# Kernel optimization log

Measured on AMD Instinct MI355X. Metric: run time of the kernel, lower is better.

The kernel has to match this reference:

```python
import jax, jax.numpy as jnp
import numpy as np
import math

B = 2
D_MODEL = 2048
L_MAX = 4096
FILTER_ORDER = 64
EMB_DIM = 3
SHORT_K = 3


def setup_inputs() -> dict:
    key = jax.random.key(0)
    ks = jax.random.split(key, 16)
    D = D_MODEL

    def n(k, shape, scale=0.02):
        return jax.random.normal(k, shape, dtype=jnp.float32) * scale

    return {
        "x": jax.random.normal(ks[0], (B, L_MAX, D), dtype=jnp.float32),
        "in_proj_w": n(ks[1], (3 * D, D)),
        "in_proj_b": n(ks[2], (3 * D,)),
        "short_w": n(ks[3], (3 * D, 1, SHORT_K), 0.3),   # depthwise conv weight (O, I/groups=1, K)
        "short_b": n(ks[4], (3 * D,), 0.1),
        "mlp_w0": n(ks[5], (FILTER_ORDER, EMB_DIM), 0.5),
        "mlp_b0": n(ks[6], (FILTER_ORDER,), 0.5),
        "sin_freq": jnp.ones((1, FILTER_ORDER), dtype=jnp.float32),  # Sin module, w=1, shared across MLP layers
        "mlp_w1": n(ks[7], (FILTER_ORDER, FILTER_ORDER), 0.1),
        "mlp_b1": n(ks[8], (FILTER_ORDER,), 0.1),
        "mlp_w2": n(ks[9], (FILTER_ORDER, FILTER_ORDER), 0.1),
        "mlp_b2": n(ks[10], (FILTER_ORDER,), 0.1),
        "mlp_w3": n(ks[11], (D, FILTER_ORDER), 0.1),      # final Linear(order -> d_model, bias=False)
        "filter_bias": jax.random.normal(ks[12], (D,), dtype=jnp.float32),  # HyenaFilter.bias ~ randn
        "out_proj_w": n(ks[13], (D, D)),
        "out_proj_b": n(ks[14], (D,)),
    }


def _pos_emb(L):
    # PositionalEmbedding: t in [0,1], 1 complex band (emb_dim=3 -> bands=1)
    t = jnp.linspace(0.0, 1.0, L)[:, None]               # (L, 1)
    t_resc = jnp.linspace(0.0, L - 1.0, L)
    w = 2.0 * math.pi * t_resc / L                       # (L,)
    bands = (EMB_DIM - 1) // 2
    f = jnp.linspace(1e-4, bands - 1.0, bands)           # (bands,)
    ang = f[None, :] * w[:, None]                        # (L, bands)
    # z = exp(-1j * f * w) -> real = cos, imag = -sin
    z = jnp.concatenate([t, jnp.cos(ang), -jnp.sin(ang)], axis=-1)  # (L, 3)
    return z, t


def _filter_k(L, w0, b0, freq, w1, b1, w2, b2, w3):
    z, t = _pos_emb(L)
    h = jnp.sin(freq * (z @ w0.T + b0))
    h = jnp.sin(freq * (h @ w1.T + b1))
    h = jnp.sin(freq * (h @ w2.T + b2))
    h = h @ w3.T                                         # (L, D)
    # ExponentialModulation: deltas = linspace(log(.01)/1.5, log(.01)/0.3, D)
    max_decay = math.log(0.01) / 0.3
    min_decay = math.log(0.01) / 1.5
    deltas = jnp.linspace(min_decay, max_decay, h.shape[-1])
    decay = jnp.exp(-t * jnp.abs(deltas)[None, :])       # (L, D)
    return (h * decay).T                                 # (D, L)


def _fftconv(u, k, bias):
    # fftconv_ref with gelu=False, no dropout_mask: u (B, D, L), k (D, L), bias (D,)
    L = u.shape[-1]
    n = 2 * L
    k_f = jnp.fft.rfft(k, n=n) / n                       # (D, L+1)
    u_f = jnp.fft.rfft(u, n=n)                           # (B, D, L+1)
    y = jnp.fft.irfft(u_f * k_f, n=n, norm="forward")[..., :L]
    return y + u * bias[:, None]


def reference(x, in_proj_w, in_proj_b, short_w, short_b, mlp_w0, mlp_b0, sin_freq,
              mlp_w1, mlp_b1, mlp_w2, mlp_b2, mlp_w3, filter_bias,
              out_proj_w, out_proj_b):
    Bn, L, D = x.shape
    u = x @ in_proj_w.T + in_proj_b                      # (B, L, 3D)
    u = jnp.transpose(u, (0, 2, 1))                      # (B, 3D, L)
    # depthwise short conv, padding = short_k - 1, truncate to L (causal-ish)
    uc = jax.lax.conv_general_dilated(
        u, short_w, window_strides=(1,),
        padding=[(SHORT_K - 1, SHORT_K - 1)],
        feature_group_count=3 * D,
        dimension_numbers=("NCH", "OIH", "NCH"))
    uc = uc[..., :L] + short_b[None, :, None]
    x0, x1, v = jnp.split(uc, 3, axis=1)                 # each (B, D, L)
    k = _filter_k(L, mlp_w0, mlp_b0, sin_freq, mlp_w1, mlp_b1, mlp_w2, mlp_b2, mlp_w3)
    # order=2 Hyena recurrence: single gated long-conv step
    v = v * x1
    v = _fftconv(v, k, filter_bias)
    y = v * x0                                           # (B, D, L)
    y = jnp.transpose(y, (0, 2, 1))                      # (B, L, D)
    return y @ out_proj_w.T + out_proj_b
```

## Files before the change

### kernel.cpp

```cpp
#include <hip/hip_runtime.h>
#include <hip/hip_bf16.h>
#include <cstdint>
#include <cstddef>

typedef __attribute__((ext_vector_type(8))) short    bf16x8;
typedef __attribute__((ext_vector_type(4))) float    f32x4;
typedef __attribute__((ext_vector_type(8))) unsigned short u16x8;
typedef __attribute__((ext_vector_type(4))) float    f32v4;
typedef __attribute__((ext_vector_type(4))) unsigned short u16v4;

__device__ __forceinline__ float b2f(unsigned short v) {
    return __builtin_bit_cast(float, ((unsigned int)v) << 16);
}
__device__ __forceinline__ unsigned short f2b(float f) {
    unsigned int u = __builtin_bit_cast(unsigned int, f);
    u += 0x7fffu + ((u >> 16) & 1u);
    return (unsigned short)(u >> 16);
}

__device__ __forceinline__ void async16(const void* g, void* l) {
    __builtin_amdgcn_global_load_lds(
        (const __attribute__((address_space(1))) unsigned int*)g,
        (__attribute__((address_space(3))) unsigned int*)l, 16, 0, 0);
}

__global__ __launch_bounds__(256) void cvt2_f32_bf16(
    const float* __restrict__ srcA, unsigned short* __restrict__ dstA, int n4A,
    const float* __restrict__ srcB, unsigned short* __restrict__ dstB, int n4B) {
    int i = blockIdx.x * blockDim.x + threadIdx.x;
    int stride = gridDim.x * blockDim.x;
    const int nTot = n4A + n4B;
    for (; i < nTot; i += stride) {
        const bool inA = (i < n4A);
        const f32v4* s4 = inA ? (const f32v4*)srcA : (const f32v4*)srcB;
        u16v4* d4 = inA ? (u16v4*)dstA : (u16v4*)dstB;
        const int k = inA ? i : (i - n4A);
        f32v4 v = s4[k];
        u16v4 o;
        o.x = f2b(v.x); o.y = f2b(v.y); o.z = f2b(v.z); o.w = f2b(v.w);
        d4[k] = o;
    }
}

__global__ __launch_bounds__(256) void cvt_f32_bf16(const float* __restrict__ src,
                                                    unsigned short* __restrict__ dst, int n4) {
    int i = blockIdx.x * blockDim.x + threadIdx.x;
    int stride = gridDim.x * blockDim.x;
    const f32v4* s4 = (const f32v4*)src;
    u16v4* d4 = (u16v4*)dst;
    for (; i < n4; i += stride) {
        f32v4 v = s4[i];
        u16v4 o;
        o.x = f2b(v.x); o.y = f2b(v.y); o.z = f2b(v.z); o.w = f2b(v.w);
        d4[i] = o;
    }
}

template <int MODE>
__global__ __launch_bounds__(512, 1) void gemm256(
    const unsigned short* __restrict__ A,
    const unsigned short* __restrict__ Bw,
    const float* __restrict__ bias,
    void* __restrict__ Cout,
    int M, int N, int K, int Lseq, int CH, int ntn)
{
    constexpr int SMEM_BYTES = (MODE == 1) ? 135168 : 131072;
    __shared__ char smemc[SMEM_BYTES];

    const int tid = threadIdx.x;
    const int w   = tid >> 6;
    const int l   = tid & 63;
    const int wm  = w & 1;
    const int wn  = w >> 1;
    const int quad = l >> 4;
    const int lq   = l & 15;

    const int bid = blockIdx.x;
    const int x  = bid & 7;
    const int j  = bid >> 3;
    const int bx = (j & 7) + 8 * (j >> 5);
    const int by = (x << 2) | ((j >> 3) & 3);
    const int n0 = bx * 256, m0 = by * 256;

    const int su0 = quad ^ (lq & 7);
    const int su1 = su0 ^ 4;

    uint32_t offAe[2][2], offBe[2][2];
    int dA[2][2], dB[2][2];
    #pragma unroll
    for (int h = 0; h < 2; ++h)
        #pragma unroll
        for (int c = 0; c < 2; ++c) {
            const int Lr = h * 128 + w * 16 + c * 8 + (l >> 3);
            const int gA = ((Lr & 64) << 1) | ((Lr & 128) >> 1) | (Lr & 63);
            const int u  = (l & 7) ^ (l >> 3);
            offAe[h][c] = (uint32_t)(m0 + gA) * (uint32_t)K + (uint32_t)(u * 8);
            offBe[h][c] = (uint32_t)(n0 + Lr) * (uint32_t)K + (uint32_t)(u * 8);
            const int rb = (h * 128 + w * 16 + c * 8) * 128;
            dA[h][c] = rb;
            dB[h][c] = 32768 + rb;
        }

#define STAGE_A(bs, h, tile) do { \
    async16(A + offAe[h][0] + (size_t)(tile) * 64, smemc + ((bs) * 65536 + dA[h][0])); \
    async16(A + offAe[h][1] + (size_t)(tile) * 64, smemc + ((bs) * 65536 + dA[h][1])); \
} while (0)
#define STAGE_B(bs, h, tile) do { \
    async16(Bw + offBe[h][0] + (size_t)(tile) * 64, smemc + ((bs) * 65536 + dB[h][0])); \
    async16(Bw + offBe[h][1] + (size_t)(tile) * 64, smemc + ((bs) * 65536 + dB[h][1])); \
} while (0)

    f32x4 acc[8][4] = {};
    bf16x8 bw[4][2], a[2][2];

#define LDB8(bs) do { \
    _Pragma("unroll") for (int jj = 0; jj < 4; ++jj) { \
        const int Lr = wn * 64 + jj * 16 + lq; \
        bw[jj][0] = *(const bf16x8*)(smemc + (bs) * 65536 + 32768 + Lr * 128 + su0 * 16); \
        bw[jj][1] = *(const bf16x8*)(smemc + (bs) * 65536 + 32768 + Lr * 128 + su1 * 16); \
    } } while (0)
#define LDA4(bs, q) do { \
    _Pragma("unroll") for (int mf = 0; mf < 2; ++mf) { \
        const int g = wm * 128 + (q) * 32 + mf * 16 + lq; \
        const int Lr = ((g & 64) << 1) | ((g & 128) >> 1) | (g & 63); \
        a[mf][0] = *(const bf16x8*)(smemc + (bs) * 65536 + Lr * 128 + su0 * 16); \
        a[mf][1] = *(const bf16x8*)(smemc + (bs) * 65536 + Lr * 128 + su1 * 16); \
    } } while (0)
#define MFMA16(q) do { \
    _Pragma("unroll") for (int mf = 0; mf < 2; ++mf) \
    _Pragma("unroll") for (int jj = 0; jj < 4; ++jj) \
    _Pragma("unroll") for (int kk = 0; kk < 2; ++kk) \
        acc[(q) * 2 + mf][jj] = __builtin_amdgcn_mfma_f32_16x16x32_bf16(a[mf][kk], bw[jj][kk], acc[(q) * 2 + mf][jj], 0, 0, 0); \
} while (0)
#define PHASE_SYNC() do { \
    __builtin_amdgcn_s_barrier(); \
    asm volatile("s_waitcnt lgkmcnt(0)" ::: "memory"); \
    __builtin_amdgcn_sched_barrier(0); \
    __builtin_amdgcn_s_setprio(1); \
} while (0)
#define PHASE_END() do { \
    __builtin_amdgcn_s_setprio(0); \
    __builtin_amdgcn_s_barrier(); \
} while (0)
#define PHASE_END_DRAIN(lastf) do { \
    __builtin_amdgcn_s_setprio(0); \
    if (lastf) asm volatile("s_waitcnt vmcnt(0)" ::: "memory"); \
    else       asm volatile("s_waitcnt vmcnt(6)" ::: "memory"); \
    __builtin_amdgcn_s_barrier(); \
} while (0)

    STAGE_B(0, 0, 0); STAGE_B(0, 1, 0); STAGE_A(0, 0, 0); STAGE_A(0, 1, 0);
    STAGE_B(1, 0, 1); STAGE_B(1, 1, 1); STAGE_A(1, 0, 1);
    asm volatile("s_waitcnt vmcnt(6)" ::: "memory");
    __builtin_amdgcn_s_barrier();

    const int nIt = K >> 7;
    for (int i = 0; i < nIt; ++i) {
        const bool last = (i == nIt - 1);
        const int t0 = 2 * i, t1 = 2 * i + 1;
        LDB8(0); LDA4(0, 0); STAGE_A(1, 1, t1);
        PHASE_SYNC(); MFMA16(0); PHASE_END();
        LDA4(0, 1); if (!last) STAGE_B(0, 0, t0 + 2);
        PHASE_SYNC(); MFMA16(1); PHASE_END();
        LDA4(0, 2); if (!last) STAGE_B(0, 1, t0 + 2);
        PHASE_SYNC(); MFMA16(2); PHASE_END();
        LDA4(0, 3); if (!last) STAGE_A(0, 0, t0 + 2);
        PHASE_SYNC(); MFMA16(3); PHASE_END_DRAIN(last);
        LDB8(1); LDA4(1, 0); if (!last) STAGE_A(0, 1, t0 + 2);
        PHASE_SYNC(); MFMA16(0); PHASE_END();
        LDA4(1, 1); if (!last) STAGE_B(1, 0, t1 + 2);
        PHASE_SYNC(); MFMA16(1); PHASE_END();
        LDA4(1, 2); if (!last) STAGE_B(1, 1, t1 + 2);
        PHASE_SYNC(); MFMA16(2); PHASE_END();
        LDA4(1, 3); if (!last) STAGE_A(1, 0, t1 + 2);
        PHASE_SYNC(); MFMA16(3); PHASE_END_DRAIN(last);
    }

    if (MODE == 0) {
        float* out = (float*)Cout;
        #pragma unroll
        for (int jj = 0; jj < 4; ++jj) {
            const int col = n0 + wn * 64 + jj * 16 + lq;
            const float bv = bias[col];
            #pragma unroll
            for (int i8 = 0; i8 < 8; ++i8) {
                const int rowb = m0 + wm * 128 + i8 * 16 + quad * 4;
                f32x4 c = acc[i8][jj];
                out[(size_t)(rowb + 0) * N + col] = c.x + bv;
                out[(size_t)(rowb + 1) * N + col] = c.y + bv;
                out[(size_t)(rowb + 2) * N + col] = c.z + bv;
                out[(size_t)(rowb + 3) * N + col] = c.w + bv;
            }
        }
    } else {
        unsigned short* sE = (unsigned short*)smemc;
        __syncthreads();
        #pragma unroll
        for (int jj = 0; jj < 4; ++jj) {
            const int nl = wn * 64 + jj * 16 + lq;
            const float bv = bias[n0 + nl];
            #pragma unroll
            for (int i8 = 0; i8 < 8; ++i8) {
                const int ml = wm * 128 + i8 * 16 + quad * 4;
                f32x4 c = acc[i8][jj];
                u16v4 pk;
                pk.x = f2b(c.x + bv); pk.y = f2b(c.y + bv);
                pk.z = f2b(c.z + bv); pk.w = f2b(c.w + bv);
                *(u16v4*)&sE[nl * 264 + ml] = pk;
            }
        }
        __syncthreads();
        unsigned short* uo = (unsigned short*)Cout;
        const int bI = m0 >> 12;
        const int l0 = m0 & 4095;
        for (int e = tid; e < 8192; e += 512) {
            const int nl = e >> 5, seg = e & 31;
            u16x8 v = *(const u16x8*)&sE[nl * 264 + seg * 8];
            *(u16x8*)&uo[(size_t)(bI * CH + n0 + nl) * Lseq + l0 + seg * 8] = v;
        }
    }
#undef STAGE_A
#undef STAGE_B
#undef LDB8
#undef LDA4
#undef MFMA16
#undef PHASE_SYNC
#undef PHASE_END
#undef PHASE_END_DRAIN
}

__global__ __launch_bounds__(256) void filter_kernel(
    const float* __restrict__ w0, const float* __restrict__ b0,
    const float* __restrict__ freq,
    const float* __restrict__ w1, const float* __restrict__ b1,
    const float* __restrict__ w2, const float* __restrict__ b2,
    const float* __restrict__ w3, float* __restrict__ kf)
{
    __shared__ float ha[64][64];
    __shared__ float hb[64][64];
    const int tid = threadIdx.x;
    const int l0 = blockIdx.x * 64;
    const int d0 = blockIdx.y * 256;
    const int l  = tid & 63;
    const int lg = l0 + l;
    const float tt = (float)lg * (1.0f / 4095.0f);
    const float wang = 6.283185307179586f * (float)lg * (1.0f / 4096.0f);
    const float a  = 1e-4f * wang;
    const float z0 = tt, z1 = cosf(a), z2 = -sinf(a);

    for (int e = tid; e < 4096; e += 256) {
        const int dim = e >> 6;
        float pre = z0 * w0[dim * 3] + z1 * w0[dim * 3 + 1] + z2 * w0[dim * 3 + 2] + b0[dim];
        ha[dim][l] = sinf(freq[dim] * pre);
    }
    __syncthreads();
    for (int e = tid; e < 4096; e += 256) {
        const int dim = e >> 6;
        float acc = b1[dim];
        #pragma unroll
        for (int jj = 0; jj < 64; ++jj) acc += w1[dim * 64 + jj] * ha[jj][l];
        hb[dim][l] = sinf(freq[dim] * acc);
    }
    __syncthreads();
    for (int e = tid; e < 4096; e += 256) {
        const int dim = e >> 6;
        float acc = b2[dim];
        #pragma unroll
        for (int jj = 0; jj < 64; ++jj) acc += w2[dim * 64 + jj] * hb[jj][l];
        ha[dim][l] = sinf(freq[dim] * acc);
    }
    __syncthreads();
    for (int d = d0 + (tid >> 6); d < d0 + 256; d += 4) {
        float acc = 0.f;
        #pragma unroll
        for (int jj = 0; jj < 64; ++jj) acc += w3[d * 64 + jj] * ha[jj][l];
        const float delta = fabsf(-3.0701134573253944f + (-5.999245642062483e-3f) * (float)d);
        kf[(size_t)d * 4096 + lg] = acc * __expf(-tt * delta);
    }
}

#define PIDX(i) ((i) + (((i) >> 5) << 2))

__device__ __forceinline__ void bfly_f(float& r1, float& i1, float& r2, float& i2, float wr, float wi) {
    float ur = r1, ui = i1, vr = r2, vi = i2;
    r1 = ur + vr; i1 = ui + vi;
    float dr = ur - vr, di = ui - vi;
    r2 = dr * wr - di * wi;
    i2 = dr * wi + di * wr;
}
__device__ __forceinline__ void bfly_i(float& r1, float& i1, float& r2, float& i2, float wr, float wi) {
    float vr = r2 * wr - i2 * wi, vi = r2 * wi + i2 * wr;
    float ur = r1, ui = i1;
    r1 = ur + vr; i1 = ui + vi;
    r2 = ur - vr; i2 = ui - vi;
}

template <int DS, int STR>
__device__ __forceinline__ void fwd_stage(float* re, float* im, int tt) {
    float wr[8], wi[8];
    constexpr float c = -3.14159265358979f / (float)(STR * DS);
    #pragma unroll
    for (int k = 0; k < DS; ++k) __sincosf(c * (float)(tt + STR * k), &wi[k], &wr[k]);
    #pragma unroll
    for (int s = 0; s < 16; ++s)
        if ((s & DS) == 0)
            bfly_f(re[s], im[s], re[s + DS], im[s + DS], wr[s & (DS - 1)], wi[s & (DS - 1)]);
}
template <int DS, int STR>
__device__ __forceinline__ void inv_stage(float* re, float* im, int tt) {
    float wr[8], wi[8];
    constexpr float c = 3.14159265358979f / (float)(STR * DS);
    #pragma unroll
    for (int k = 0; k < DS; ++k) __sincosf(c * (float)(tt + STR * k), &wi[k], &wr[k]);
    #pragma unroll
    for (int s = 0; s < 16; ++s)
        if ((s & DS) == 0)
            bfly_i(re[s], im[s], re[s + DS], im[s + DS], wr[s & (DS - 1)], wi[s & (DS - 1)]);
}

__device__ constexpr float TW8C[8] = { 1.f,  0.9238795325112867f,  0.7071067811865476f,  0.3826834323650898f,
                                       0.f, -0.3826834323650898f, -0.7071067811865476f, -0.9238795325112867f };
__device__ constexpr float TW8S[8] = { 0.f,  0.3826834323650898f,  0.7071067811865476f,  0.9238795325112867f,
                                       1.f,  0.9238795325112867f,  0.7071067811865476f,  0.3826834323650898f };
template <int DS>
__device__ __forceinline__ void fwd_stageC(float* re, float* im) {
    #pragma unroll
    for (int s = 0; s < 16; ++s)
        if ((s & DS) == 0) {
            const int k = (s & (DS - 1)) * (8 / DS);
            bfly_f(re[s], im[s], re[s + DS], im[s + DS], TW8C[k], -TW8S[k]);
        }
}
template <int DS>
__device__ __forceinline__ void inv_stageC(float* re, float* im) {
    #pragma unroll
    for (int s = 0; s < 16; ++s)
        if ((s & DS) == 0) {
            const int k = (s & (DS - 1)) * (8 / DS);
            bfly_i(re[s], im[s], re[s + DS], im[s + DS], TW8C[k], TW8S[k]);
        }
}

__device__ __forceinline__ void xchg(float* re, float* im, float* fre, float* fim,
                                     int wbase, int wstr, int rbase, int rstr) {
    __syncthreads();
    if (wstr == 1) {
        #pragma unroll
        for (int q = 0; q < 4; ++q) {
            f32x4 vr, vi;
            vr.x = re[4*q+0]; vr.y = re[4*q+1]; vr.z = re[4*q+2]; vr.w = re[4*q+3];
            vi.x = im[4*q+0]; vi.y = im[4*q+1]; vi.z = im[4*q+2]; vi.w = im[4*q+3];
            *(f32x4*)&fre[PIDX(wbase + 4*q)] = vr;
            *(f32x4*)&fim[PIDX(wbase + 4*q)] = vi;
        }
    } else {
        #pragma unroll
        for (int s = 0; s < 16; ++s) {
            const int i = wbase + wstr * s;
            fre[PIDX(i)] = re[s]; fim[PIDX(i)] = im[s];
        }
    }
    __syncthreads();
    if (rstr == 1) {
        #pragma unroll
        for (int q = 0; q < 4; ++q) {
            f32x4 vr = *(const f32x4*)&fre[PIDX(rbase + 4*q)];
            f32x4 vi = *(const f32x4*)&fim[PIDX(rbase + 4*q)];
            re[4*q+0] = vr.x; re[4*q+1] = vr.y; re[4*q+2] = vr.z; re[4*q+3] = vr.w;
            im[4*q+0] = vi.x; im[4*q+1] = vi.y; im[4*q+2] = vi.z; im[4*q+3] = vi.w;
        }
    } else {
        #pragma unroll
        for (int s = 0; s < 16; ++s) {
            const int i = rbase + rstr * s;
            re[s] = fre[PIDX(i)]; im[s] = fim[PIDX(i)];
        }
    }
}

__device__ __forceinline__ void fwd_fft(float* re, float* im, float* fre, float* fim, int t) {
    const int off = t & 31, seg = t >> 5;
    fwd_stage<8, 512>(re, im, t);
    fwd_stage<4, 512>(re, im, t);
    fwd_stage<2, 512>(re, im, t);
    fwd_stage<1, 512>(re, im, t);
    xchg(re, im, fre, fim, t, 512, seg * 512 + off, 32);
    fwd_stage<8, 32>(re, im, off);
    fwd_stage<4, 32>(re, im, off);
    fwd_stage<2, 32>(re, im, off);
    fwd_stage<1, 32>(re, im, off);
    {
        float wr, wi;
        __sincosf(-3.14159265358979f * (float)(off & 15) / 16.0f, &wi, &wr);
        const bool hi = (off & 16) != 0;
        #pragma unroll
        for (int s = 0; s < 16; ++s) {
            float rr = __shfl_xor(re[s], 16);
            float ri = __shfl_xor(im[s], 16);
            if (!hi) { re[s] += rr; im[s] += ri; }
            else {
                float dr = rr - re[s], di = ri - im[s];
                re[s] = dr * wr - di * wi;
                im[s] = dr * wi + di * wr;
            }
        }
    }
    xchg(re, im, fre, fim, seg * 512 + off, 32, 16 * t, 1);
    fwd_stageC<8>(re, im);
    fwd_stageC<4>(re, im);
    fwd_stageC<2>(re, im);
    fwd_stageC<1>(re, im);
}

__device__ __forceinline__ void inv_fft(float* re, float* im, float* fre, float* fim, int t) {
    const int off = t & 31, seg = t >> 5;
    inv_stageC<1>(re, im);
    inv_stageC<2>(re, im);
    inv_stageC<4>(re, im);
    inv_stageC<8>(re, im);
    xchg(re, im, fre, fim, 16 * t, 1, seg * 512 + off, 32);
    {
        float wr, wi;
        __sincosf(3.14159265358979f * (float)(off & 15) / 16.0f, &wi, &wr);
        const bool hi = (off & 16) != 0;
        #pragma unroll
        for (int s = 0; s < 16; ++s) {
            float rr = __shfl_xor(re[s], 16);
            float ri = __shfl_xor(im[s], 16);
            if (!hi) {
                float vr = rr * wr - ri * wi, vi = rr * wi + ri * wr;
                re[s] += vr; im[s] += vi;
            } else {
                float vr = re[s] * wr - im[s] * wi, vi = re[s] * wi + im[s] * wr;
                re[s] = rr - vr; im[s] = ri - vi;
            }
        }
    }
    inv_stage<1, 32>(re, im, off);
    inv_stage<2, 32>(re, im, off);
    inv_stage<4, 32>(re, im, off);
    inv_stage<8, 32>(re, im, off);
    xchg(re, im, fre, fim, seg * 512 + off, 32, t, 512);
    inv_stage<1, 512>(re, im, t);
    inv_stage<2, 512>(re, im, t);
    inv_stage<4, 512>(re, im, t);
    inv_stage<8, 512>(re, im, t);
}

struct ConvPre { u16x8 v; float m1, m2; };
__device__ __forceinline__ ConvPre conv_pre(const unsigned short* __restrict__ row, int lb) {
    ConvPre p;
    p.v  = *(const u16x8*)(row + lb);
    p.m1 = (lb >= 1) ? b2f(row[lb - 1]) : 0.f;
    p.m2 = (lb >= 2) ? b2f(row[lb - 2]) : 0.f;
    return p;
}
__device__ __forceinline__ void conv_do(const ConvPre& p,
                                        float W0, float W1, float W2, float BB,
                                        float* __restrict__ out) {
    float f[8];
    #pragma unroll
    for (int j = 0; j < 8; ++j) f[j] = b2f((unsigned short)p.v[j]);
    out[0] = W0 * p.m2 + W1 * p.m1 + W2 * f[0] + BB;
    out[1] = W0 * p.m1 + W1 * f[0] + W2 * f[1] + BB;
    #pragma unroll
    for (int j = 2; j < 8; ++j) out[j] = W0 * f[j - 2] + W1 * f[j - 1] + W2 * f[j] + BB;
}

__global__ __launch_bounds__(512, 2) void hyena_fft_kernel(
    const unsigned short* __restrict__ u,
    const float* __restrict__ kf,
    const float* __restrict__ sw,
    const float* __restrict__ sbv,
    const float* __restrict__ fbias,
    unsigned short* __restrict__ zb)
{
    __shared__ __align__(16) float fre[9216];
    __shared__ __align__(16) float fim[9216];
    const int t = threadIdx.x;
    const int d = blockIdx.x;
    const int lb = t << 3;

    const int c0 = d, c1 = 2048 + d, c2 = 4096 + d;
    const float w10 = sw[c1*3+0], w11 = sw[c1*3+1], w12 = sw[c1*3+2], bb1 = sbv[c1];
    const float w20 = sw[c2*3+0], w21 = sw[c2*3+1], w22 = sw[c2*3+2], bb2 = sbv[c2];
    const float fb = fbias[d];

    ConvPre p1[2], p2[2];
    #pragma unroll
    for (int b = 0; b < 2; ++b) {
        const size_t base = (size_t)b * 6144 * 4096;
        p1[b] = conv_pre(u + base + (size_t)c1 * 4096, lb);
        p2[b] = conv_pre(u + base + (size_t)c2 * 4096, lb);
    }

    float kr[16], ki[16];
    #pragma unroll
    for (int s = 0; s < 16; ++s) {
        kr[s] = (s < 8) ? kf[(size_t)d * 4096 + t + 512 * s] : 0.f;
        ki[s] = 0.f;
    }
    fwd_fft(kr, ki, fre, fim, t);

    float vgc[2][8];
    #pragma unroll
    for (int b = 0; b < 2; ++b) {
        float e_[8], g_[8];
        conv_do(p1[b], w10, w11, w12, bb1, e_);
        conv_do(p2[b], w20, w21, w22, bb2, g_);
        #pragma unroll
        for (int j = 0; j < 8; ++j) vgc[b][j] = g_[j] * e_[j];
    }

    __syncthreads();
    #pragma unroll
    for (int q = 0; q < 2; ++q) {
        f32x4 vr, vi;
        vr.x = vgc[0][4*q+0]; vr.y = vgc[0][4*q+1]; vr.z = vgc[0][4*q+2]; vr.w = vgc[0][4*q+3];
        vi.x = vgc[1][4*q+0]; vi.y = vgc[1][4*q+1]; vi.z = vgc[1][4*q+2]; vi.w = vgc[1][4*q+3];
        *(f32x4*)&fre[PIDX(lb + 4*q)] = vr;
        *(f32x4*)&fim[PIDX(lb + 4*q)] = vi;
    }
    __syncthreads();
    float xr[16], xi[16];
    #pragma unroll
    for (int s = 0; s < 8; ++s) {
        xr[s] = fre[PIDX(t + (s << 9))];
        xi[s] = fim[PIDX(t + (s << 9))];
    }
    #pragma unroll
    for (int s = 8; s < 16; ++s) { xr[s] = 0.f; xi[s] = 0.f; }

    fwd_fft(xr, xi, fre, fim, t);
    #pragma unroll
    for (int j = 0; j < 16; ++j) {
        const float cr = xr[j], ci = xi[j];
        xr[j] = cr * kr[j] - ci * ki[j];
        xi[j] = cr * ki[j] + ci * kr[j];
    }

    ConvPre p0[2];
    #pragma unroll
    for (int b = 0; b < 2; ++b)
        p0[b] = conv_pre(u + (size_t)b * 6144 * 4096 + (size_t)c0 * 4096, lb);

    inv_fft(xr, xi, fre, fim, t);

    __syncthreads();
    #pragma unroll
    for (int s = 0; s < 8; ++s) {
        fre[PIDX(t + (s << 9))] = xr[s];
        fim[PIDX(t + (s << 9))] = xi[s];
    }
    __syncthreads();
    float yr[8], yi[8];
    #pragma unroll
    for (int q = 0; q < 2; ++q) {
        f32x4 vr = *(const f32x4*)&fre[PIDX(lb + 4*q)];
        f32x4 vi = *(const f32x4*)&fim[PIDX(lb + 4*q)];
        yr[4*q+0] = vr.x; yr[4*q+1] = vr.y; yr[4*q+2] = vr.z; yr[4*q+3] = vr.w;
        yi[4*q+0] = vi.x; yi[4*q+1] = vi.y; yi[4*q+2] = vi.z; yi[4*q+3] = vi.w;
    }
    const float w00 = sw[c0*3+0], w01 = sw[c0*3+1], w02 = sw[c0*3+2], bb0 = sbv[c0];
    const float inv_n = 1.0f / 8192.0f;
    #pragma unroll
    for (int b = 0; b < 2; ++b) {
        float a_[8];
        conv_do(p0[b], w00, w01, w02, bb0, a_);
        const float* Y = (b == 0) ? yr : yi;
        u16x8 zv;
        #pragma unroll
        for (int j = 0; j < 8; ++j)
            zv[j] = (unsigned short)f2b((Y[j] * inv_n + vgc[b][j] * fb) * a_[j]);
        *(u16x8*)&zb[(size_t)(b * 2048 + d) * 4096 + lb] = zv;
    }
}

__global__ __launch_bounds__(256) void transpose_kernel(const unsigned short* __restrict__ zb,
                                                        unsigned short* __restrict__ zt)
{
    __shared__ unsigned int tile[64][65];
    const int l0 = blockIdx.x * 64, d0 = blockIdx.y * 64, b = blockIdx.z;
    const int tid = threadIdx.x;
    for (int e = tid; e < 4096; e += 256) {
        const int r = e >> 6, c = e & 63;
        tile[r][c] = zb[(size_t)(b * 2048 + d0 + r) * 4096 + l0 + c];
    }
    __syncthreads();
    for (int e = tid; e < 4096; e += 256) {
        const int r = e >> 6, c = e & 63;
        zt[(size_t)(b * 4096 + l0 + r) * 2048 + d0 + c] = (unsigned short)tile[c][r];
    }
}

extern "C" void kernel_launch(void* const* d_in, const int* in_sizes, int n_in,
                              void* d_out, int out_size, void* d_ws, size_t ws_size,
                              hipStream_t stream)
{
    const float* x   = (const float*)d_in[0];
    const float* ipw = (const float*)d_in[1];
    const float* ipb = (const float*)d_in[2];
    const float* sw  = (const float*)d_in[3];
    const float* sb  = (const float*)d_in[4];
    const float* w0  = (const float*)d_in[5];
    const float* b0  = (const float*)d_in[6];
    const float* fr  = (const float*)d_in[7];
    const float* w1  = (const float*)d_in[8];
    const float* b1  = (const float*)d_in[9];
    const float* w2  = (const float*)d_in[10];
    const float* b2  = (const float*)d_in[11];
    const float* w3  = (const float*)d_in[12];
    const float* fb  = (const float*)d_in[13];
    const float* opw = (const float*)d_in[14];
    const float* opb = (const float*)d_in[15];
    float* out = (float*)d_out;

    char* ws = (char*)d_ws;
    unsigned short* xb  = (unsigned short*)ws;
    unsigned short* wbi = (unsigned short*)(ws + 33554432);
    unsigned short* zbm = (unsigned short*)ws;
    unsigned short* ztb = (unsigned short*)(ws + 33554432);
    unsigned short* wbo = (unsigned short*)(ws + 67108864);
    unsigned short* ub  = (unsigned short*)(ws + 134217728);
    float*          kf  = (float*)(ws + 234881024);

    cvt2_f32_bf16<<<1536, 256, 0, stream>>>(x, xb, 16777216 / 4, ipw, wbi, 12582912 / 4);

    gemm256<1><<<768, 512, 0, stream>>>(xb, wbi, ipb, ub, 8192, 6144, 2048, 4096, 6144, 24);

    filter_kernel<<<dim3(64, 8), 256, 0, stream>>>(w0, b0, fr, w1, b1, w2, b2, w3, kf);

    cvt_f32_bf16<<<512, 256, 0, stream>>>(opw, wbo, 4194304 / 4);

    hyena_fft_kernel<<<2048, 512, 0, stream>>>(ub, kf, sw, sb, fb, zbm);

    transpose_kernel<<<dim3(64, 32, 2), 256, 0, stream>>>(zbm, ztb);

    gemm256<0><<<256, 512, 0, stream>>>(ztb, wbo, opb, out, 8192, 2048, 2048, 4096, 2048, 8);
}
```

Measured before the change: 737.0 us.

## Cut FFT kernel LDS and registers, recompute gates, fold weight convert

The FFT kernel's LDS padding shrinks from 4 floats per 32 to 1 float per 32, so the shared arrays drop from 9216 to 8448 floats. The vectorized LDS exchange paths are replaced with scalar strided accesses. The gate values v*x1 are no longer held in registers across the FFTs; their inputs are reloaded and recomputed at the end, which lowers register pressure at the cost of extra global reads. The out_proj weight conversion is merged into the single input-conversion launch, removing one kernel launch.

After: 754.7 us. 2.4% more time.

```diff
diff --git a/kernel.cpp b/kernel.cpp
--- a/kernel.cpp
+++ b/kernel.cpp
@@ -24,35 +24,22 @@
         (__attribute__((address_space(3))) unsigned int*)l, 16, 0, 0);
 }
 
-__global__ __launch_bounds__(256) void cvt2_f32_bf16(
+__global__ __launch_bounds__(256) void cvt3_f32_bf16(
     const float* __restrict__ srcA, unsigned short* __restrict__ dstA, int n4A,
-    const float* __restrict__ srcB, unsigned short* __restrict__ dstB, int n4B) {
+    const float* __restrict__ srcB, unsigned short* __restrict__ dstB, int n4B,
+    const float* __restrict__ srcC, unsigned short* __restrict__ dstC, int n4C) {
     int i = blockIdx.x * blockDim.x + threadIdx.x;
     int stride = gridDim.x * blockDim.x;
-    const int nTot = n4A + n4B;
+    const int nAB = n4A + n4B, nTot = nAB + n4C;
     for (; i < nTot; i += stride) {
-        const bool inA = (i < n4A);
-        const f32v4* s4 = inA ? (const f32v4*)srcA : (const f32v4*)srcB;
-        u16v4* d4 = inA ? (u16v4*)dstA : (u16v4*)dstB;
-        const int k = inA ? i : (i - n4A);
+        const f32v4* s4; u16v4* d4; int k;
+        if (i < n4A)      { s4 = (const f32v4*)srcA; d4 = (u16v4*)dstA; k = i; }
+        else if (i < nAB) { s4 = (const f32v4*)srcB; d4 = (u16v4*)dstB; k = i - n4A; }
+        else              { s4 = (const f32v4*)srcC; d4 = (u16v4*)dstC; k = i - nAB; }
         f32v4 v = s4[k];
         u16v4 o;
         o.x = f2b(v.x); o.y = f2b(v.y); o.z = f2b(v.z); o.w = f2b(v.w);
         d4[k] = o;
-    }
-}
-
-__global__ __launch_bounds__(256) void cvt_f32_bf16(const float* __restrict__ src,
-                                                    unsigned short* __restrict__ dst, int n4) {
-    int i = blockIdx.x * blockDim.x + threadIdx.x;
-    int stride = gridDim.x * blockDim.x;
-    const f32v4* s4 = (const f32v4*)src;
-    u16v4* d4 = (u16v4*)dst;
-    for (; i < n4; i += stride) {
-        f32v4 v = s4[i];
-        u16v4 o;
-        o.x = f2b(v.x); o.y = f2b(v.y); o.z = f2b(v.z); o.w = f2b(v.w);
-        d4[i] = o;
     }
 }
 
@@ -279,7 +266,7 @@
     }
 }
 
-#define PIDX(i) ((i) + (((i) >> 5) << 2))
+#define PIDX(i) ((i) + ((i) >> 5))
 
 __device__ __forceinline__ void bfly_f(float& r1, float& i1, float& r2, float& i2, float wr, float wi) {
     float ur = r1, ui = i1, vr = r2, vi = i2;
@@ -344,37 +331,16 @@
 __device__ __forceinline__ void xchg(float* re, float* im, float* fre, float* fim,
                                      int wbase, int wstr, int rbase, int rstr) {
     __syncthreads();
-    if (wstr == 1) {
-        #pragma unroll
-        for (int q = 0; q < 4; ++q) {
-            f32x4 vr, vi;
-            vr.x = re[4*q+0]; vr.y = re[4*q+1]; vr.z = re[4*q+2]; vr.w = re[4*q+3];
-            vi.x = im[4*q+0]; vi.y = im[4*q+1]; vi.z = im[4*q+2]; vi.w = im[4*q+3];
-            *(f32x4*)&fre[PIDX(wbase + 4*q)] = vr;
-            *(f32x4*)&fim[PIDX(wbase + 4*q)] = vi;
-        }
-    } else {
-        #pragma unroll
-        for (int s = 0; s < 16; ++s) {
-            const int i = wbase + wstr * s;
-            fre[PIDX(i)] = re[s]; fim[PIDX(i)] = im[s];
-        }
-    }
-    __syncthreads();
-    if (rstr == 1) {
-        #pragma unroll
-        for (int q = 0; q < 4; ++q) {
-            f32x4 vr = *(const f32x4*)&fre[PIDX(rbase + 4*q)];
-            f32x4 vi = *(const f32x4*)&fim[PIDX(rbase + 4*q)];
-            re[4*q+0] = vr.x; re[4*q+1] = vr.y; re[4*q+2] = vr.z; re[4*q+3] = vr.w;
-            im[4*q+0] = vi.x; im[4*q+1] = vi.y; im[4*q+2] = vi.z; im[4*q+3] = vi.w;
-        }
-    } else {
-        #pragma unroll
-        for (int s = 0; s < 16; ++s) {
-            const int i = rbase + rstr * s;
-            re[s] = fre[PIDX(i)]; im[s] = fim[PIDX(i)];
-        }
+    #pragma unroll
+    for (int s = 0; s < 16; ++s) {
+        const int i = wbase + wstr * s;
+        fre[PIDX(i)] = re[s]; fim[PIDX(i)] = im[s];
+    }
+    __syncthreads();
+    #pragma unroll
+    for (int s = 0; s < 16; ++s) {
+        const int i = rbase + rstr * s;
+        re[s] = fre[PIDX(i)]; im[s] = fim[PIDX(i)];
     }
 }
 
@@ -475,16 +441,13 @@
     const float* __restrict__ fbias,
     unsigned short* __restrict__ zb)
 {
-    __shared__ __align__(16) float fre[9216];
-    __shared__ __align__(16) float fim[9216];
+    __shared__ float fre[8448];
+    __shared__ float fim[8448];
     const int t = threadIdx.x;
     const int d = blockIdx.x;
     const int lb = t << 3;
 
     const int c0 = d, c1 = 2048 + d, c2 = 4096 + d;
-    const float w10 = sw[c1*3+0], w11 = sw[c1*3+1], w12 = sw[c1*3+2], bb1 = sbv[c1];
-    const float w20 = sw[c2*3+0], w21 = sw[c2*3+1], w22 = sw[c2*3+2], bb2 = sbv[c2];
-    const float fb = fbias[d];
 
     ConvPre p1[2], p2[2];
     #pragma unroll
@@ -502,24 +465,27 @@
     }
     fwd_fft(kr, ki, fre, fim, t);
 
-    float vgc[2][8];
-    #pragma unroll
-    for (int b = 0; b < 2; ++b) {
-        float e_[8], g_[8];
-        conv_do(p1[b], w10, w11, w12, bb1, e_);
-        conv_do(p2[b], w20, w21, w22, bb2, g_);
-        #pragma unroll
-        for (int j = 0; j < 8; ++j) vgc[b][j] = g_[j] * e_[j];
-    }
-
-    __syncthreads();
-    #pragma unroll
-    for (int q = 0; q < 2; ++q) {
-        f32x4 vr, vi;
-        vr.x = vgc[0][4*q+0]; vr.y = vgc[0][4*q+1]; vr.z = vgc[0][4*q+2]; vr.w = vgc[0][4*q+3];
-        vi.x = vgc[1][4*q+0]; vi.y = vgc[1][4*q+1]; vi.z = vgc[1][4*q+2]; vi.w = vgc[1][4*q+3];
-        *(f32x4*)&fre[PIDX(lb + 4*q)] = vr;
-        *(f32x4*)&fim[PIDX(lb + 4*q)] = vi;
+    {
+        const float w10 = sw[c1*3+0], w11 = sw[c1*3+1], w12 = sw[c1*3+2], bb1 = sbv[c1];
+        const float w20 = sw[c2*3+0], w21 = sw[c2*3+1], w22 = sw[c2*3+2], bb2 = sbv[c2];
+        float vg0[8], vg1[8];
+        {
+            float e_[8], g_[8];
+            conv_do(p1[0], w10, w11, w12, bb1, e_);
+            conv_do(p2[0], w20, w21, w22, bb2, g_);
+            #pragma unroll
+            for (int j = 0; j < 8; ++j) vg0[j] = g_[j] * e_[j];
+            conv_do(p1[1], w10, w11, w12, bb1, e_);
+            conv_do(p2[1], w20, w21, w22, bb2, g_);
+            #pragma unroll
+            for (int j = 0; j < 8; ++j) vg1[j] = g_[j] * e_[j];
+        }
+        __syncthreads();
+        #pragma unroll
+        for (int j = 0; j < 8; ++j) {
+            fre[PIDX(lb + j)] = vg0[j];
+            fim[PIDX(lb + j)] = vg1[j];
+        }
     }
     __syncthreads();
     float xr[16], xi[16];
@@ -539,10 +505,14 @@
         xi[j] = cr * ki[j] + ci * kr[j];
     }
 
-    ConvPre p0[2];
-    #pragma unroll
-    for (int b = 0; b < 2; ++b)
-        p0[b] = conv_pre(u + (size_t)b * 6144 * 4096 + (size_t)c0 * 4096, lb);
+    ConvPre q0[2], q1[2], q2[2];
+    #pragma unroll
+    for (int b = 0; b < 2; ++b) {
+        const size_t base = (size_t)b * 6144 * 4096;
+        q0[b] = conv_pre(u + base + (size_t)c0 * 4096, lb);
+        q1[b] = conv_pre(u + base + (size_t)c1 * 4096, lb);
+        q2[b] = conv_pre(u + base + (size_t)c2 * 4096, lb);
+    }
 
     inv_fft(xr, xi, fre, fim, t);
 
@@ -553,25 +523,24 @@
         fim[PIDX(t + (s << 9))] = xi[s];
     }
     __syncthreads();
-    float yr[8], yi[8];
-    #pragma unroll
-    for (int q = 0; q < 2; ++q) {
-        f32x4 vr = *(const f32x4*)&fre[PIDX(lb + 4*q)];
-        f32x4 vi = *(const f32x4*)&fim[PIDX(lb + 4*q)];
-        yr[4*q+0] = vr.x; yr[4*q+1] = vr.y; yr[4*q+2] = vr.z; yr[4*q+3] = vr.w;
-        yi[4*q+0] = vi.x; yi[4*q+1] = vi.y; yi[4*q+2] = vi.z; yi[4*q+3] = vi.w;
-    }
     const float w00 = sw[c0*3+0], w01 = sw[c0*3+1], w02 = sw[c0*3+2], bb0 = sbv[c0];
+    const float w10 = sw[c1*3+0], w11 = sw[c1*3+1], w12 = sw[c1*3+2], bb1 = sbv[c1];
+    const float w20 = sw[c2*3+0], w21 = sw[c2*3+1], w22 = sw[c2*3+2], bb2 = sbv[c2];
+    const float fb = fbias[d];
     const float inv_n = 1.0f / 8192.0f;
     #pragma unroll
     for (int b = 0; b < 2; ++b) {
-        float a_[8];
-        conv_do(p0[b], w00, w01, w02, bb0, a_);
-        const float* Y = (b == 0) ? yr : yi;
+        float a_[8], e_[8], g_[8];
+        conv_do(q0[b], w00, w01, w02, bb0, a_);
+        conv_do(q1[b], w10, w11, w12, bb1, e_);
+        conv_do(q2[b], w20, w21, w22, bb2, g_);
+        const float* Y = (b == 0) ? fre : fim;
         u16x8 zv;
         #pragma unroll
-        for (int j = 0; j < 8; ++j)
-            zv[j] = (unsigned short)f2b((Y[j] * inv_n + vgc[b][j] * fb) * a_[j]);
+        for (int j = 0; j < 8; ++j) {
+            const float y = Y[PIDX(lb + j)];
+            zv[j] = (unsigned short)f2b((y * inv_n + g_[j] * e_[j] * fb) * a_[j]);
+        }
         *(u16x8*)&zb[(size_t)(b * 2048 + d) * 4096 + lb] = zv;
     }
 }
@@ -624,14 +593,14 @@
     unsigned short* ub  = (unsigned short*)(ws + 134217728);
     float*          kf  = (float*)(ws + 234881024);
 
-    cvt2_f32_bf16<<<1536, 256, 0, stream>>>(x, xb, 16777216 / 4, ipw, wbi, 12582912 / 4);
+    cvt3_f32_bf16<<<2048, 256, 0, stream>>>(x, xb, 16777216 / 4,
+                                            ipw, wbi, 12582912 / 4,
+                                            opw, wbo, 4194304 / 4);
 
     gemm256<1><<<768, 512, 0, stream>>>(xb, wbi, ipb, ub, 8192, 6144, 2048, 4096, 6144, 24);
 
     filter_kernel<<<dim3(64, 8), 256, 0, stream>>>(w0, b0, fr, w1, b1, w2, b2, w3, kf);
 
-    cvt_f32_bf16<<<512, 256, 0, stream>>>(opw, wbo, 4194304 / 4);
-
     hyena_fft_kernel<<<2048, 512, 0, stream>>>(ub, kf, sw, sb, fb, zbm);
 
     transpose_kernel<<<dim3(64, 32, 2), 256, 0, stream>>>(zbm, ztb);
```
